# Kernel optimization log

Measured on AMD Instinct MI355X. Metric: run time of the kernel, lower is better.

## Reference

```python
import jax, jax.numpy as jnp
import numpy as np

B, S, DIM = 4, 4096, 1024
H, HD = 16, 64  # n_heads, head_dim = dim // n_heads
UMV = 20.0      # unified_max_value (init kwarg)


def setup_inputs() -> dict:
    key = jax.random.key(0)
    kx, kw = jax.random.split(key)
    x = jax.random.normal(kx, (B, S, DIM), dtype=jnp.float32)
    # qkv_proj: Linear(dim, 3*dim). Small weight scale + positive bias keeps
    # attention scores inside the keep-window [0, 2*UMV] so denominators are safe.
    W_qkv = jax.random.normal(kw, (DIM, 3 * DIM), dtype=jnp.float32) * 0.02
    b_qkv = jnp.full((3 * DIM,), 0.5, dtype=jnp.float32)
    return {"x": x, "W_qkv": W_qkv, "b_qkv": b_qkv}


def reference(x, W_qkv, b_qkv):
    Bb, Ss, _ = x.shape
    qkv = x @ W_qkv + b_qkv                      # [B,S,3*dim]
    qkv = qkv.reshape(Bb, Ss, H, 3 * HD)          # [B,S,H,3*hd]
    Q, K, V = jnp.split(qkv, 3, axis=-1)          # each [B,S,H,hd]
    # matmul(Q, K.transpose(-2,-1)) on [B,S,H,hd]: contract head_dim -> [B,S,H,H]
    s = jnp.einsum('bshd,bsgd->bshg', Q, K) - UMV
    e = jnp.exp(s)
    mask = (s > UMV) | (s < -UMV)                 # keep only s in [-UMV, UMV]
    e = jnp.where(mask, 0.0, e)
    denom = jnp.sum(e, axis=-1, keepdims=True)
    p = e / denom                                  # [B,S,H,H]
    out = jnp.einsum('bshg,bsgd->bshd', p, V)      # [B,S,H,hd]
    return out
```

## Files before the change

kernel.cpp:

```cpp
#include <hip/hip_runtime.h>

typedef _Float16 v8h __attribute__((ext_vector_type(8)));
typedef _Float16 v4h __attribute__((ext_vector_type(4)));
typedef _Float16 v2h __attribute__((ext_vector_type(2)));
typedef float v4f __attribute__((ext_vector_type(4)));

__device__ __forceinline__ void gl16(const void* g, void* l) {
    __builtin_amdgcn_global_load_lds(
        (const __attribute__((address_space(1))) unsigned int*)g,
        (__attribute__((address_space(3))) unsigned int*)l, 16, 0, 0);
}

__global__ __launch_bounds__(256) void k_cvt_x(const float* __restrict__ x,
                                               _Float16* __restrict__ x16) {
    int i = (blockIdx.x * 256 + threadIdx.x) * 8;
    float4 a = *(const float4*)(x + i);
    float4 b = *(const float4*)(x + i + 4);
    v8h h;
    h[0] = (_Float16)a.x; h[1] = (_Float16)a.y; h[2] = (_Float16)a.z; h[3] = (_Float16)a.w;
    h[4] = (_Float16)b.x; h[5] = (_Float16)b.y; h[6] = (_Float16)b.z; h[7] = (_Float16)b.w;
    *(v8h*)(x16 + i) = h;
}

__global__ __launch_bounds__(256) void k_cvt_w(const float* __restrict__ W,
                                               _Float16* __restrict__ Wt) {
    __shared__ float T[64][68];
    int k0 = (blockIdx.x & 15) * 64;
    int n0 = (blockIdx.x >> 4) * 64;
    int t = threadIdx.x;
    int tr = t >> 4;
    int tc = t & 15;
#pragma unroll
    for (int rr = 0; rr < 4; rr++) {
        int kk = rr * 16 + tr;
        float4 v = *(const float4*)(W + (size_t)(k0 + kk) * 3072 + n0 + tc * 4);
        T[kk][tc * 4 + 0] = v.x; T[kk][tc * 4 + 1] = v.y;
        T[kk][tc * 4 + 2] = v.z; T[kk][tc * 4 + 3] = v.w;
    }
    __syncthreads();
#pragma unroll
    for (int ww = 0; ww < 4; ww++) {
        int nn = ww * 16 + tr;
        v4h h;
#pragma unroll
        for (int i = 0; i < 4; i++) h[i] = (_Float16)T[tc * 4 + i][nn];
        *(v4h*)(Wt + (size_t)(n0 + nn) * 1024 + k0 + tc * 4) = h;
    }
}

__global__ __launch_bounds__(256) void k_gemm(const _Float16* __restrict__ A,
                                              const _Float16* __restrict__ Bt,
                                              const float* __restrict__ bias,
                                              _Float16* __restrict__ C) {
    __shared__ __align__(16) _Float16 As[128 * 32];
    __shared__ __align__(16) _Float16 Bs[128 * 32];
    int bm = blockIdx.x & 127;
    int bn = blockIdx.x >> 7;
    int m0 = bm * 128, n0 = bn * 128;
    int tid = threadIdx.x;
    int w = tid >> 6, lane = tid & 63;
    int quad = lane >> 4, l15 = lane & 15;
    int wm = (w & 1) * 64, wn = (w >> 1) * 64;

    int mc1 = w * 16 + (lane >> 2);
    int mc2 = (w + 4) * 16 + (lane >> 2);
    int k8 = (lane & 3) * 8;
    const _Float16* aS1 = A + (size_t)(m0 + mc1) * 1024 + k8;
    const _Float16* aS2 = A + (size_t)(m0 + mc2) * 1024 + k8;
    const _Float16* bS1 = Bt + (size_t)(n0 + mc1) * 1024 + k8;
    const _Float16* bS2 = Bt + (size_t)(n0 + mc2) * 1024 + k8;
    _Float16* lA1 = &As[w * 512];
    _Float16* lA2 = &As[(w + 4) * 512];
    _Float16* lB1 = &Bs[w * 512];
    _Float16* lB2 = &Bs[(w + 4) * 512];

    v4f acc[4][4] = {};

    for (int kt = 0; kt < 1024; kt += 32) {
        __syncthreads();
        gl16(aS1 + kt, lA1);
        gl16(aS2 + kt, lA2);
        gl16(bS1 + kt, lB1);
        gl16(bS2 + kt, lB2);
        __syncthreads();
        v8h af[4], bf[4];
#pragma unroll
        for (int mi = 0; mi < 4; mi++)
            af[mi] = *(const v8h*)&As[(wm + mi * 16 + l15) * 32 + quad * 8];
#pragma unroll
        for (int ni = 0; ni < 4; ni++)
            bf[ni] = *(const v8h*)&Bs[(wn + ni * 16 + l15) * 32 + quad * 8];
#pragma unroll
        for (int mi = 0; mi < 4; mi++)
#pragma unroll
            for (int ni = 0; ni < 4; ni++)
                acc[mi][ni] = __builtin_amdgcn_mfma_f32_16x16x32_f16(af[mi], bf[ni], acc[mi][ni], 0, 0, 0);
    }

#pragma unroll
    for (int ni = 0; ni < 4; ni++) {
        int n = n0 + wn + ni * 16 + l15;
        float bv = bias[n];
#pragma unroll
        for (int mi = 0; mi < 4; mi++) {
            int mbase = m0 + wm + mi * 16 + quad * 4;
#pragma unroll
            for (int r = 0; r < 4; r++)
                C[(size_t)(mbase + r) * 3072 + n] = (_Float16)(acc[mi][ni][r] + bv);
        }
    }
}

__global__ __launch_bounds__(256) void k_attn(const _Float16* __restrict__ qkv,
                                              float* __restrict__ out) {
    __shared__ __align__(16) _Float16 Lh[4][16 * 200];
    __shared__ float Pb[4][16 * 17];
    int tid = threadIdx.x;
    int w = tid >> 6, lane = tid & 63;
    int pos = blockIdx.x * 4 + w;
    _Float16* L = Lh[w];
    float* P = Pb[w];
    const _Float16* src = qkv + (size_t)pos * 3072;

#pragma unroll
    for (int ii = 0; ii < 6; ii++) {
        int e = (ii * 64 + lane) * 8;
        v8h v = *(const v8h*)(src + e);
        int h = e / 192, r = e % 192;
        *(v8h*)(L + h * 200 + r) = v;
    }
    __syncthreads();

    {
        int h = lane & 15, quad = lane >> 4;
        const _Float16* Qr = L + h * 200;
        v8h q[8];
#pragma unroll
        for (int d = 0; d < 8; d++) q[d] = *(const v8h*)(Qr + d * 8);
        float e4[4];
#pragma unroll
        for (int c = 0; c < 4; c++) {
            const _Float16* Kr = L + (quad * 4 + c) * 200 + 64;
            float a = 0.f;
#pragma unroll
            for (int d = 0; d < 8; d++) {
                v8h k = *(const v8h*)(Kr + d * 8);
#pragma unroll
                for (int j = 0; j < 4; j++)
                    a = __builtin_amdgcn_fdot2(((v2h*)&q[d])[j], ((v2h*)&k)[j], a, false);
            }
            float s = a - 20.0f;
            e4[c] = (s > 20.0f || s < -20.0f) ? 0.0f : __expf(s);
        }
        float part = e4[0] + e4[1] + e4[2] + e4[3];
        part += __shfl_xor(part, 16, 64);
        part += __shfl_xor(part, 32, 64);
        float inv = 1.0f / part;
#pragma unroll
        for (int c = 0; c < 4; c++) P[h * 17 + quad * 4 + c] = e4[c] * inv;
    }
    __syncthreads();

    {
        int h2 = lane >> 2, db = (lane & 3) * 16;
        float o[16];
#pragma unroll
        for (int i = 0; i < 16; i++) o[i] = 0.f;
#pragma unroll
        for (int g = 0; g < 16; g++) {
            float p = P[h2 * 17 + g];
            const _Float16* Vr = L + g * 200 + 128 + db;
            v8h v0 = *(const v8h*)(Vr);
            v8h v1 = *(const v8h*)(Vr + 8);
#pragma unroll
            for (int i = 0; i < 8; i++) {
                o[i]     += p * (float)v0[i];
                o[8 + i] += p * (float)v1[i];
            }
        }
        float* dst = out + (size_t)pos * 1024 + h2 * 64 + db;
#pragma unroll
        for (int d4 = 0; d4 < 4; d4++) {
            float4 v;
            v.x = o[d4 * 4 + 0]; v.y = o[d4 * 4 + 1];
            v.z = o[d4 * 4 + 2]; v.w = o[d4 * 4 + 3];
            *(float4*)(dst + d4 * 4) = v;
        }
    }
}

extern "C" void kernel_launch(void* const* d_in, const int* in_sizes, int n_in,
                              void* d_out, int out_size, void* d_ws, size_t ws_size,
                              hipStream_t stream) {
    (void)in_sizes; (void)n_in; (void)out_size; (void)ws_size;
    const float* x  = (const float*)d_in[0];
    const float* Wq = (const float*)d_in[1];
    const float* bq = (const float*)d_in[2];
    float* out = (float*)d_out;

    char* ws = (char*)d_ws;
    _Float16* x16   = (_Float16*)ws;
    _Float16* wt16  = (_Float16*)(ws + (32u << 20));
    _Float16* qkv16 = (_Float16*)(ws + (38u << 20));

    k_cvt_x<<<8192, 256, 0, stream>>>(x, x16);
    k_cvt_w<<<768, 256, 0, stream>>>(Wq, wt16);
    k_gemm<<<3072, 256, 0, stream>>>(x16, wt16, bq, qkv16);
    k_attn<<<4096, 256, 0, stream>>>(qkv16, out);
}
```

Baseline: 283.8 us.

## Double-buffer GEMM A tile, load B directly, merge convert kernels, relax attn syncs

Fuses the two fp16 conversion kernels into one launch. The GEMM now double-buffers only the A tile in LDS, prefetching the next k-slice while computing, and reads B fragments straight from global memory into registers, so one barrier per iteration is removed. The attention kernel replaces block barriers with a per-wave LDS waitcnt, since each wave works only on its own LDS slice. Risks: direct global B loads are uncoalesced and add latency, and the wave-only fence relies on the compiler keeping LDS ordering within a wave.

```diff
diff --git a/kernel.cpp b/kernel.cpp
--- a/kernel.cpp
+++ b/kernel.cpp
@@ -11,40 +11,46 @@
         (__attribute__((address_space(3))) unsigned int*)l, 16, 0, 0);
 }
 
-__global__ __launch_bounds__(256) void k_cvt_x(const float* __restrict__ x,
-                                               _Float16* __restrict__ x16) {
-    int i = (blockIdx.x * 256 + threadIdx.x) * 8;
-    float4 a = *(const float4*)(x + i);
-    float4 b = *(const float4*)(x + i + 4);
-    v8h h;
-    h[0] = (_Float16)a.x; h[1] = (_Float16)a.y; h[2] = (_Float16)a.z; h[3] = (_Float16)a.w;
-    h[4] = (_Float16)b.x; h[5] = (_Float16)b.y; h[6] = (_Float16)b.z; h[7] = (_Float16)b.w;
-    *(v8h*)(x16 + i) = h;
-}
-
-__global__ __launch_bounds__(256) void k_cvt_w(const float* __restrict__ W,
-                                               _Float16* __restrict__ Wt) {
-    __shared__ float T[64][68];
-    int k0 = (blockIdx.x & 15) * 64;
-    int n0 = (blockIdx.x >> 4) * 64;
-    int t = threadIdx.x;
-    int tr = t >> 4;
-    int tc = t & 15;
-#pragma unroll
-    for (int rr = 0; rr < 4; rr++) {
-        int kk = rr * 16 + tr;
-        float4 v = *(const float4*)(W + (size_t)(k0 + kk) * 3072 + n0 + tc * 4);
-        T[kk][tc * 4 + 0] = v.x; T[kk][tc * 4 + 1] = v.y;
-        T[kk][tc * 4 + 2] = v.z; T[kk][tc * 4 + 3] = v.w;
-    }
-    __syncthreads();
-#pragma unroll
-    for (int ww = 0; ww < 4; ww++) {
-        int nn = ww * 16 + tr;
-        v4h h;
-#pragma unroll
-        for (int i = 0; i < 4; i++) h[i] = (_Float16)T[tc * 4 + i][nn];
-        *(v4h*)(Wt + (size_t)(n0 + nn) * 1024 + k0 + tc * 4) = h;
+__device__ __forceinline__ void wave_lds_fence() {
+    asm volatile("s_waitcnt lgkmcnt(0)" ::: "memory");
+}
+
+__global__ __launch_bounds__(256) void k_cvt(const float* __restrict__ x,
+                                             _Float16* __restrict__ x16,
+                                             const float* __restrict__ W,
+                                             _Float16* __restrict__ Wt) {
+    if (blockIdx.x < 8192) {
+        int i = (blockIdx.x * 256 + threadIdx.x) * 8;
+        float4 a = *(const float4*)(x + i);
+        float4 b = *(const float4*)(x + i + 4);
+        v8h h;
+        h[0] = (_Float16)a.x; h[1] = (_Float16)a.y; h[2] = (_Float16)a.z; h[3] = (_Float16)a.w;
+        h[4] = (_Float16)b.x; h[5] = (_Float16)b.y; h[6] = (_Float16)b.z; h[7] = (_Float16)b.w;
+        *(v8h*)(x16 + i) = h;
+    } else {
+        __shared__ float T[64][68];
+        int bid = blockIdx.x - 8192;
+        int k0 = (bid & 15) * 64;
+        int n0 = (bid >> 4) * 64;
+        int t = threadIdx.x;
+        int tr = t >> 4;
+        int tc = t & 15;
+#pragma unroll
+        for (int rr = 0; rr < 4; rr++) {
+            int kk = rr * 16 + tr;
+            float4 v = *(const float4*)(W + (size_t)(k0 + kk) * 3072 + n0 + tc * 4);
+            T[kk][tc * 4 + 0] = v.x; T[kk][tc * 4 + 1] = v.y;
+            T[kk][tc * 4 + 2] = v.z; T[kk][tc * 4 + 3] = v.w;
+        }
+        __syncthreads();
+#pragma unroll
+        for (int ww = 0; ww < 4; ww++) {
+            int nn = ww * 16 + tr;
+            v4h h;
+#pragma unroll
+            for (int i = 0; i < 4; i++) h[i] = (_Float16)T[tc * 4 + i][nn];
+            *(v4h*)(Wt + (size_t)(n0 + nn) * 1024 + k0 + tc * 4) = h;
+        }
     }
 }
 
@@ -52,8 +58,7 @@
                                               const _Float16* __restrict__ Bt,
                                               const float* __restrict__ bias,
                                               _Float16* __restrict__ C) {
-    __shared__ __align__(16) _Float16 As[128 * 32];
-    __shared__ __align__(16) _Float16 Bs[128 * 32];
+    __shared__ __align__(16) _Float16 As[2][128 * 32];
     int bm = blockIdx.x & 127;
     int bn = blockIdx.x >> 7;
     int m0 = bm * 128, n0 = bn * 128;
@@ -62,34 +67,36 @@
     int quad = lane >> 4, l15 = lane & 15;
     int wm = (w & 1) * 64, wn = (w >> 1) * 64;
 
-    int mc1 = w * 16 + (lane >> 2);
-    int mc2 = (w + 4) * 16 + (lane >> 2);
-    int k8 = (lane & 3) * 8;
-    const _Float16* aS1 = A + (size_t)(m0 + mc1) * 1024 + k8;
-    const _Float16* aS2 = A + (size_t)(m0 + mc2) * 1024 + k8;
-    const _Float16* bS1 = Bt + (size_t)(n0 + mc1) * 1024 + k8;
-    const _Float16* bS2 = Bt + (size_t)(n0 + mc2) * 1024 + k8;
-    _Float16* lA1 = &As[w * 512];
-    _Float16* lA2 = &As[(w + 4) * 512];
-    _Float16* lB1 = &Bs[w * 512];
-    _Float16* lB2 = &Bs[(w + 4) * 512];
+    int idx1 = tid, idx2 = 256 + tid;
+    const _Float16* aG1 = A + (size_t)(m0 + (idx1 >> 2)) * 1024 + (idx1 & 3) * 8;
+    const _Float16* aG2 = A + (size_t)(m0 + (idx2 >> 2)) * 1024 + (idx2 & 3) * 8;
+
+    const _Float16* bR[4];
+#pragma unroll
+    for (int ni = 0; ni < 4; ni++)
+        bR[ni] = Bt + (size_t)(n0 + wn + ni * 16 + l15) * 1024 + quad * 8;
 
     v4f acc[4][4] = {};
 
-    for (int kt = 0; kt < 1024; kt += 32) {
+    gl16(aG1, &As[0][idx1 * 8]);
+    gl16(aG2, &As[0][idx2 * 8]);
+
+    for (int it = 0; it < 32; it++) {
         __syncthreads();
-        gl16(aS1 + kt, lA1);
-        gl16(aS2 + kt, lA2);
-        gl16(bS1 + kt, lB1);
-        gl16(bS2 + kt, lB2);
-        __syncthreads();
+        int cur = it & 1;
+        if (it < 31) {
+            int ko = (it + 1) * 32;
+            gl16(aG1 + ko, &As[cur ^ 1][idx1 * 8]);
+            gl16(aG2 + ko, &As[cur ^ 1][idx2 * 8]);
+        }
+        int kt = it * 32;
         v8h af[4], bf[4];
 #pragma unroll
         for (int mi = 0; mi < 4; mi++)
-            af[mi] = *(const v8h*)&As[(wm + mi * 16 + l15) * 32 + quad * 8];
+            af[mi] = *(const v8h*)&As[cur][(wm + mi * 16 + l15) * 32 + quad * 8];
 #pragma unroll
         for (int ni = 0; ni < 4; ni++)
-            bf[ni] = *(const v8h*)&Bs[(wn + ni * 16 + l15) * 32 + quad * 8];
+            bf[ni] = *(const v8h*)(bR[ni] + kt);
 #pragma unroll
         for (int mi = 0; mi < 4; mi++)
 #pragma unroll
@@ -129,7 +136,7 @@
         int h = e / 192, r = e % 192;
         *(v8h*)(L + h * 200 + r) = v;
     }
-    __syncthreads();
+    wave_lds_fence();
 
     {
         int h = lane & 15, quad = lane >> 4;
@@ -159,7 +166,7 @@
 #pragma unroll
         for (int c = 0; c < 4; c++) P[h * 17 + quad * 4 + c] = e4[c] * inv;
     }
-    __syncthreads();
+    wave_lds_fence();
 
     {
         int h2 = lane >> 2, db = (lane & 3) * 16;
@@ -203,8 +210,7 @@
     _Float16* wt16  = (_Float16*)(ws + (32u << 20));
     _Float16* qkv16 = (_Float16*)(ws + (38u << 20));
 
-    k_cvt_x<<<8192, 256, 0, stream>>>(x, x16);
-    k_cvt_w<<<768, 256, 0, stream>>>(Wq, wt16);
+    k_cvt<<<8960, 256, 0, stream>>>(x, x16, Wq, wt16);
     k_gemm<<<3072, 256, 0, stream>>>(x16, wt16, bq, qkv16);
     k_attn<<<4096, 256, 0, stream>>>(qkv16, out);
 }
```

Result: slower. 377.5 us (+33.0%).
